# Optimization experiments

Hardware: AMD Instinct MI355X
Metric: run time of the kernel (lower is better)

The kernel has to match this reference:

```python
import jax, jax.numpy as jnp
import numpy as np
from jax import lax

C = 256
HEADS = 8
HEAD_DIM = C // HEADS
B, H, W = 16, 32, 32
EPS = 1e-5


def conv3x3(x, w, b):
    # x: [B,C,H,W], w: [O,I,3,3]
    y = lax.conv_general_dilated(x, w, (1, 1), 'SAME',
                                 dimension_numbers=('NCHW', 'OIHW', 'NCHW'))
    return y + b[None, :, None, None]


def conv1x1(x, w, b):
    # w: [O,C]; pointwise conv as einsum
    return jnp.einsum('oc,bchw->bohw', w, x) + b[None, :, None, None]


def batchnorm(x, gamma, beta, mean, var):
    inv = gamma / jnp.sqrt(var + EPS)
    return x * inv[None, :, None, None] + (beta - mean * inv)[None, :, None, None]


def setup_inputs() -> dict:
    key = jax.random.key(0)
    ks = jax.random.split(key, 16)
    s3 = 1.0 / np.sqrt(C * 9)
    s1 = 1.0 / np.sqrt(C)
    return {
        'x': jax.random.normal(ks[0], (B, C, H, W), jnp.float32),
        'conv1_w': jax.random.normal(ks[1], (C, C, 3, 3), jnp.float32) * s3,
        'conv1_b': jnp.zeros((C,), jnp.float32),
        'bn1_gamma': jnp.ones((C,), jnp.float32),
        'bn1_beta': jnp.zeros((C,), jnp.float32),
        'bn1_mean': jax.random.normal(ks[2], (C,), jnp.float32) * 0.1,
        'bn1_var': jax.random.uniform(ks[3], (C,), jnp.float32, 0.5, 1.5),
        'conv2_w': jax.random.normal(ks[4], (C, C, 3, 3), jnp.float32) * s3,
        'conv2_b': jnp.zeros((C,), jnp.float32),
        'bn2_gamma': jnp.ones((C,), jnp.float32),
        'bn2_beta': jnp.zeros((C,), jnp.float32),
        'bn2_mean': jax.random.normal(ks[5], (C,), jnp.float32) * 0.1,
        'bn2_var': jax.random.uniform(ks[6], (C,), jnp.float32, 0.5, 1.5),
        'q_w': jax.random.normal(ks[7], (C, C), jnp.float32) * s1,
        'q_b': jnp.zeros((C,), jnp.float32),
        'k_w': jax.random.normal(ks[8], (C, C), jnp.float32) * s1,
        'k_b': jnp.zeros((C,), jnp.float32),
        'v_w': jax.random.normal(ks[9], (C, C), jnp.float32) * s1,
        'v_b': jnp.zeros((C,), jnp.float32),
        'out_w': jax.random.normal(ks[10], (C, C), jnp.float32) * s1,
        'out_b': jnp.zeros((C,), jnp.float32),
        'gate': jnp.asarray(0.1, jnp.float32),
    }


def reference(x, conv1_w, conv1_b, bn1_gamma, bn1_beta, bn1_mean, bn1_var,
              conv2_w, conv2_b, bn2_gamma, bn2_beta, bn2_mean, bn2_var,
              q_w, q_b, k_w, k_b, v_w, v_b, out_w, out_b, gate):
    b, c, h, w = x.shape
    n = h * w
    residual = x
    # conv residual path
    conv_out = jax.nn.relu(batchnorm(conv3x3(x, conv1_w, conv1_b),
                                     bn1_gamma, bn1_beta, bn1_mean, bn1_var))
    conv_out = batchnorm(conv3x3(conv_out, conv2_w, conv2_b),
                         bn2_gamma, bn2_beta, bn2_mean, bn2_var)
    # spatial multi-head attention (eval mode: dropout is identity)
    q = conv1x1(x, q_w, q_b).reshape(b, HEADS, HEAD_DIM, n)
    k = conv1x1(x, k_w, k_b).reshape(b, HEADS, HEAD_DIM, n)
    v = conv1x1(x, v_w, v_b).reshape(b, HEADS, HEAD_DIM, n)
    scores = jnp.einsum('bhdn,bhdm->bhnm', q, k) / np.sqrt(HEAD_DIM).astype(np.float32)
    attn = jax.nn.softmax(scores, axis=-1)  # [B,heads,N,N]
    attn_out = jnp.einsum('bhdm,bhnm->bhdn', v, attn).reshape(b, c, h, w)
    attn_out = conv1x1(attn_out, out_w, out_b)
    out = conv_out + jax.nn.sigmoid(gate) * attn_out + residual
    return jax.nn.relu(out)
```

## Files before the change

kernel.cpp:

```cpp
#include <hip/hip_runtime.h>
#include <hip/hip_bf16.h>

using bf16 = __hip_bfloat16;
typedef __attribute__((ext_vector_type(4))) float floatx4;
typedef __attribute__((ext_vector_type(8))) __bf16 bf16x8;
typedef __attribute__((ext_vector_type(4))) __bf16 bf16x4;

#define LGKM_WAIT() asm volatile("s_waitcnt lgkmcnt(0)" ::: "memory")

__device__ __forceinline__ void prep_one(const float* __restrict__ src,
                                         bf16* __restrict__ dst, int idx, int ntaps)
{
    const int kk = idx & 31, o = (idx >> 5) & 255, kc = (idx >> 13) & 7, t = idx >> 16;
    dst[idx] = __float2bfloat16(src[(o * 256 + kc * 32 + kk) * ntaps + t]);
}

__global__ __launch_bounds__(256) void prep_all(
    const float* __restrict__ x,
    const float* __restrict__ w1, const float* __restrict__ w2,
    const float* __restrict__ qw, const float* __restrict__ kw,
    const float* __restrict__ vw, const float* __restrict__ ow,
    bf16* __restrict__ xk, bf16* __restrict__ w1f, bf16* __restrict__ w2f,
    bf16* __restrict__ qwf, bf16* __restrict__ kwf,
    bf16* __restrict__ vwf, bf16* __restrict__ owf)
{
    __shared__ float T[64][65];
    const int blk = blockIdx.x, tid = threadIdx.x;
    if (blk < 1024) {
        const int n0 = (blk & 15) * 64, c0 = ((blk >> 4) & 3) * 64, b = blk >> 6;
        #pragma unroll
        for (int it = 0; it < 4; ++it) {
            const int tau = tid + it * 256;
            const int c = tau >> 4, seg = tau & 15;
            const float4 vv = *(const float4*)&x[((b * 256 + c0 + c) << 10) + n0 + seg * 4];
            T[seg * 4 + 0][c] = vv.x; T[seg * 4 + 1][c] = vv.y;
            T[seg * 4 + 2][c] = vv.z; T[seg * 4 + 3][c] = vv.w;
        }
        __syncthreads();
        #pragma unroll
        for (int it = 0; it < 2; ++it) {
            const int tau = tid + it * 256;
            const int n = tau >> 3, seg = tau & 7;
            bf16x8 o8;
            #pragma unroll
            for (int q = 0; q < 8; ++q) o8[q] = (__bf16)T[n][seg * 8 + q];
            const int c = c0 + seg * 8;
            *(bf16x8*)&xk[((((b << 3) + (c >> 5)) << 10) + n0 + n) * 32 + (c & 31)] = o8;
        }
    } else if (blk < 2176) {
        const int base = (blk - 1024) * 256 + tid;
        #pragma unroll
        for (int k = 0; k < 4; ++k) {
            const int idx = base + k * 294912;
            if (idx < 589824) prep_one(w1, w1f, idx, 9);
            else              prep_one(w2, w2f, idx - 589824, 9);
        }
    } else {
        const int r = (blk - 2176) * 256 + tid;
        prep_one(qw, qwf, r, 1);
        prep_one(kw, kwf, r, 1);
        prep_one(vw, vwf, r, 1);
        prep_one(ow, owf, r, 1);
    }
}

template<int MODE>
__device__ __forceinline__ void conv_body(
    unsigned char* smb, int bn, int bo, int b,
    const bf16* __restrict__ Wf, const bf16* __restrict__ Act,
    const float* __restrict__ bias,
    const float* __restrict__ gam, const float* __restrict__ bet,
    const float* __restrict__ mu, const float* __restrict__ var,
    void* __restrict__ outp)
{
    const int tid = threadIdx.x;
    const int wave = tid >> 6, lane = tid & 63;
    const int quad = lane >> 4, l16 = lane & 15;
    const int wm = wave & 1, wn = wave >> 1;

    int srow[4], scol[4], sn[4]; bool sval[4];
    #pragma unroll
    for (int it = 0; it < 4; ++it) {
        const int s = tid + it * 256;
        const int row = s >> 2;
        const int yi = row / 34, x34 = row - yi * 34;
        const int gy = bn * 4 - 1 + yi, gx = x34 - 1;
        sval[it] = (s < 816) & (gy >= 0) & (gy < 32) & (gx >= 0) & (gx < 32);
        sn[it] = (gy << 5) + gx;
        srow[it] = row; scol[it] = (s & 3) * 8;
    }

    const bf16* __restrict__ act0 = Act + ((size_t)b << 18);
    bf16x8 rg[4];
    #pragma unroll
    for (int it = 0; it < 4; ++it) {
        bf16x8 v = {};
        if (sval[it]) v = *(const bf16x8*)&act0[sn[it] * 32 + scol[it]];
        rg[it] = v;
    }
    {
        bf16* st = (bf16*)smb;
        #pragma unroll
        for (int it = 0; it < 4; ++it)
            if (tid + it * 256 < 816) *(bf16x8*)&st[srow[it] * 40 + scol[it]] = rg[it];
    }
    __syncthreads();

    floatx4 acc[4][2] = {};

    for (int kc = 0; kc < 8; ++kc) {
        if (kc < 7) {
            const bf16* __restrict__ actn = act0 + ((kc + 1) << 15);
            #pragma unroll
            for (int it = 0; it < 4; ++it) {
                bf16x8 v = {};
                if (sval[it]) v = *(const bf16x8*)&actn[sn[it] * 32 + scol[it]];
                rg[it] = v;
            }
        }
        const bf16* __restrict__ cur = (const bf16*)(smb + (kc & 1) * 16320);
        #pragma unroll
        for (int t = 0; t < 9; ++t) {
            const int dy = t / 3 - 1, dx = t % 3 - 1;
            bf16x8 af[4], wf[2];
            #pragma unroll
            for (int p = 0; p < 4; ++p) {
                const int m = wm * 64 + p * 16 + l16;
                const int row = ((m >> 5) + 1 + dy) * 34 + ((m & 31) + 1 + dx);
                af[p] = *(const bf16x8*)&cur[row * 40 + quad * 8];
            }
            #pragma unroll
            for (int p = 0; p < 2; ++p)
                wf[p] = *(const bf16x8*)&Wf[((((t * 8 + kc) << 8) + bo * 64 + wn * 32 + p * 16 + l16) << 5) + quad * 8];
            #pragma unroll
            for (int i = 0; i < 4; ++i)
                #pragma unroll
                for (int j = 0; j < 2; ++j)
                    acc[i][j] = __builtin_amdgcn_mfma_f32_16x16x32_bf16(af[i], wf[j], acc[i][j], 0, 0, 0);
        }
        if (kc < 7) {
            bf16* nxt = (bf16*)(smb + ((kc + 1) & 1) * 16320);
            #pragma unroll
            for (int it = 0; it < 4; ++it)
                if (tid + it * 256 < 816) *(bf16x8*)&nxt[srow[it] * 40 + scol[it]] = rg[it];
        }
        __syncthreads();
    }

    if constexpr (MODE == 0) {
        bf16* rp = (bf16*)(smb + wave * 5120);
        #pragma unroll
        for (int i = 0; i < 4; ++i)
            #pragma unroll
            for (int j = 0; j < 2; ++j) {
                const int oc = bo * 64 + wn * 32 + j * 16 + l16;
                const float inv = gam[oc] * rsqrtf(var[oc] + 1e-5f);
                const float sh = bet[oc] - mu[oc] * inv;
                const float bs = bias[oc];
                #pragma unroll
                for (int r = 0; r < 4; ++r) {
                    const float v = (acc[i][j][r] + bs) * inv + sh;
                    rp[(i * 16 + quad * 4 + r) * 40 + j * 16 + l16] =
                        __float2bfloat16(v < 0.0f ? 0.0f : v);
                }
            }
        LGKM_WAIT();
        const int kc2 = bo * 2 + wn;
        bf16* dst = (bf16*)outp + ((((size_t)b << 3) + kc2) << 15) + (bn * 128 + wm * 64) * 32;
        #pragma unroll
        for (int it = 0; it < 4; ++it) {
            const int s = it * 64 + lane;
            const int nl = s >> 2, cp = (s & 3) * 8;
            *(bf16x8*)&dst[nl * 32 + cp] = *(const bf16x8*)&rp[nl * 40 + cp];
        }
    } else {
        float* rp = (float*)(smb + wave * 8704);
        #pragma unroll
        for (int i = 0; i < 4; ++i)
            #pragma unroll
            for (int j = 0; j < 2; ++j) {
                const int oc = bo * 64 + wn * 32 + j * 16 + l16;
                const float inv = gam[oc] * rsqrtf(var[oc] + 1e-5f);
                const float sh = bet[oc] - mu[oc] * inv;
                const float bs = bias[oc];
                float4 o;
                o.x = (acc[i][j][0] + bs) * inv + sh;
                o.y = (acc[i][j][1] + bs) * inv + sh;
                o.z = (acc[i][j][2] + bs) * inv + sh;
                o.w = (acc[i][j][3] + bs) * inv + sh;
                *(float4*)&rp[(j * 16 + l16) * 68 + i * 16 + quad * 4] = o;
            }
        LGKM_WAIT();
        const int n0 = bn * 128 + wm * 64;
        #pragma unroll
        for (int it = 0; it < 8; ++it) {
            const int s = it * 64 + lane;
            const int ocl = s >> 4, nch = s & 15;
            const int oc = bo * 64 + wn * 32 + ocl;
            float4 v = *(const float4*)&rp[ocl * 68 + nch * 4];
            *(float4*)&((float*)outp)[((b * 256 + oc) << 10) + n0 + nch * 4] = v;
        }
    }
}

__device__ __forceinline__ void qkv_body(
    unsigned char* qsm, int bn, int by, int b,
    const bf16* __restrict__ Wq, const bf16* __restrict__ Wk, const bf16* __restrict__ Wv,
    const bf16* __restrict__ Act,
    const float* __restrict__ bq, const float* __restrict__ bk, const float* __restrict__ bv,
    bf16* __restrict__ Oq, bf16* __restrict__ Ok, bf16* __restrict__ Ov, float qscale)
{
    const int sel = by >> 2, bo = by & 3;
    const bf16* __restrict__ Wf = (sel == 0) ? Wq : (sel == 1) ? Wk : Wv;
    const float* __restrict__ bias = (sel == 0) ? bq : (sel == 1) ? bk : bv;
    const float scale = (sel == 0) ? qscale : 1.0f;

    const int tid = threadIdx.x;
    const int wave = tid >> 6, lane = tid & 63;
    const int quad = lane >> 4, l16 = lane & 15;
    const int wm = wave & 1, wn = wave >> 1;

    floatx4 acc[4][2] = {};

    for (int kc = 0; kc < 8; ++kc) {
        const bf16* __restrict__ actk = Act + ((size_t)b << 18) + (kc << 15);
        bf16x8 af[4], wf[2];
        #pragma unroll
        for (int p = 0; p < 4; ++p)
            af[p] = *(const bf16x8*)&actk[(bn * 128 + wm * 64 + p * 16 + l16) * 32 + quad * 8];
        #pragma unroll
        for (int p = 0; p < 2; ++p)
            wf[p] = *(const bf16x8*)&Wf[(((kc << 8) + bo * 64 + wn * 32 + p * 16 + l16) << 5) + quad * 8];
        #pragma unroll
        for (int i = 0; i < 4; ++i)
            #pragma unroll
            for (int j = 0; j < 2; ++j)
                acc[i][j] = __builtin_amdgcn_mfma_f32_16x16x32_bf16(af[i], wf[j], acc[i][j], 0, 0, 0);
    }

    if (sel < 2) {
        bf16* rp = (bf16*)(qsm + wave * 5120);
        #pragma unroll
        for (int i = 0; i < 4; ++i)
            #pragma unroll
            for (int j = 0; j < 2; ++j) {
                const int oc = bo * 64 + wn * 32 + j * 16 + l16;
                const float bs = bias[oc];
                #pragma unroll
                for (int r = 0; r < 4; ++r)
                    rp[(i * 16 + quad * 4 + r) * 40 + j * 16 + l16] =
                        __float2bfloat16((acc[i][j][r] + bs) * scale);
            }
        LGKM_WAIT();
        bf16* __restrict__ outp = (sel == 0) ? Oq : Ok;
        const int h = bo * 2 + wn;
        bf16* dst = outp + ((((size_t)b << 3) + h) << 15) + (bn * 128 + wm * 64) * 32;
        #pragma unroll
        for (int it = 0; it < 4; ++it) {
            const int s = it * 64 + lane;
            const int nl = s >> 2, cp = (s & 3) * 8;
            *(bf16x8*)&dst[nl * 32 + cp] = *(const bf16x8*)&rp[nl * 40 + cp];
        }
    } else {
        bf16* rp = (bf16*)(qsm + wave * 4608);
        #pragma unroll
        for (int i = 0; i < 4; ++i)
            #pragma unroll
            for (int j = 0; j < 2; ++j) {
                const int oc = bo * 64 + wn * 32 + j * 16 + l16;
                const float bs = bias[oc];
                bf16x4 o4;
                #pragma unroll
                for (int r = 0; r < 4; ++r) o4[r] = (__bf16)(acc[i][j][r] + bs);
                *(bf16x4*)&rp[(j * 16 + l16) * 72 + i * 16 + quad * 4] = o4;
            }
        LGKM_WAIT();
        const int n0 = bn * 128 + wm * 64;
        #pragma unroll
        for (int it = 0; it < 4; ++it) {
            const int s = it * 64 + lane;
            const int ocl = s >> 3, nch = s & 7;
            const int oc = bo * 64 + wn * 32 + ocl;
            *(bf16x8*)&Ov[((b * 256 + oc) << 10) + n0 + nch * 8] =
                *(const bf16x8*)&rp[ocl * 72 + nch * 8];
        }
    }
}

__device__ __forceinline__ void attn_body(
    unsigned char* smb, int L,
    const bf16* __restrict__ Q, const bf16* __restrict__ K,
    const bf16* __restrict__ V, bf16* __restrict__ O)
{
    bf16 (*Pl)[32][136] = (bf16 (*)[32][136])smb;

    const int h = L & 7, slot = L >> 3;
    const int b = slot & 15, qb = slot >> 4;
    const int tid = threadIdx.x;
    const int wave = tid >> 6, lane = tid & 63;
    const int quad = lane >> 4, l16 = lane & 15;

    const bf16* __restrict__ Qh = Q + ((((size_t)b << 3) + h) << 15);
    const bf16* __restrict__ Kh = K + ((((size_t)b << 3) + h) << 15);
    const int qrow0 = qb * 128 + wave * 32;

    bf16x8 qf[2];
    #pragma unroll
    for (int i = 0; i < 2; ++i)
        qf[i] = *(const bf16x8*)&Qh[(qrow0 + i * 16 + l16) * 32 + quad * 8];

    float lp[2] = {0.0f, 0.0f};
    floatx4 oacc[2][2] = {};

    for (int kt = 0; kt < 8; ++kt) {
        bf16x8 kf[8];
        #pragma unroll
        for (int kb = 0; kb < 8; ++kb)
            kf[kb] = *(const bf16x8*)&Kh[(kt * 128 + kb * 16 + l16) * 32 + quad * 8];
        bf16x8 vb[2][4];
        #pragma unroll
        for (int jd = 0; jd < 2; ++jd)
            #pragma unroll
            for (int kk = 0; kk < 4; ++kk)
                vb[jd][kk] = *(const bf16x8*)&V[((b * 256 + h * 32 + jd * 16 + l16) << 10)
                                               + kt * 128 + kk * 32 + quad * 8];

        #pragma unroll
        for (int kb = 0; kb < 8; ++kb) {
            #pragma unroll
            for (int i = 0; i < 2; ++i) {
                floatx4 zz = {0.f, 0.f, 0.f, 0.f};
                floatx4 st = __builtin_amdgcn_mfma_f32_16x16x32_bf16(kf[kb], qf[i], zz, 0, 0, 0);
                const float e0 = __builtin_amdgcn_exp2f(st[0]);
                const float e1 = __builtin_amdgcn_exp2f(st[1]);
                const float e2 = __builtin_amdgcn_exp2f(st[2]);
                const float e3 = __builtin_amdgcn_exp2f(st[3]);
                lp[i] += (e0 + e1) + (e2 + e3);
                bf16x4 p4 = {(__bf16)e0, (__bf16)e1, (__bf16)e2, (__bf16)e3};
                *(bf16x4*)&Pl[wave][i * 16 + l16][kb * 16 + quad * 4] = p4;
            }
        }

        #pragma unroll
        for (int kk = 0; kk < 4; ++kk) {
            bf16x8 pf[2];
            #pragma unroll
            for (int i = 0; i < 2; ++i)
                pf[i] = *(const bf16x8*)&Pl[wave][i * 16 + l16][kk * 32 + quad * 8];
            #pragma unroll
            for (int jd = 0; jd < 2; ++jd)
                #pragma unroll
                for (int i = 0; i < 2; ++i)
                    oacc[jd][i] = __builtin_amdgcn_mfma_f32_16x16x32_bf16(
                        vb[jd][kk], pf[i], oacc[jd][i], 0, 0, 0);
        }
    }

    bf16* __restrict__ Oh = O + ((((size_t)b << 3) + h) << 15);
    #pragma unroll
    for (int i = 0; i < 2; ++i) {
        float l = lp[i];
        l += __shfl_xor(l, 16, 64);
        l += __shfl_xor(l, 32, 64);
        const float inv = 1.0f / l;
        const int qn = qrow0 + i * 16 + l16;
        #pragma unroll
        for (int jd = 0; jd < 2; ++jd) {
            bf16x4 o4;
            #pragma unroll
            for (int r = 0; r < 4; ++r) o4[r] = (__bf16)(oacc[jd][i][r] * inv);
            *(bf16x4*)&Oh[qn * 32 + jd * 16 + quad * 4] = o4;
        }
    }
}

__global__ __launch_bounds__(256) void phase1_k(
    const bf16* __restrict__ w1f, const bf16* __restrict__ xk,
    const float* __restrict__ cb1,
    const float* __restrict__ g1, const float* __restrict__ be1,
    const float* __restrict__ mu1, const float* __restrict__ va1,
    bf16* __restrict__ y1k,
    const bf16* __restrict__ qwf, const bf16* __restrict__ kwf, const bf16* __restrict__ vwf,
    const float* __restrict__ qb_, const float* __restrict__ kb_, const float* __restrict__ vb_,
    bf16* __restrict__ qT, bf16* __restrict__ kT, bf16* __restrict__ vbuf, float qscale)
{
    __shared__ __align__(16) unsigned char smb[34816];
    const int L = blockIdx.x;
    if (L < 512) {
        const int bn = L & 7, bo = (L >> 3) & 3, b = L >> 5;
        conv_body<0>(smb, bn, bo, b, w1f, xk, cb1, g1, be1, mu1, va1, (void*)y1k);
    } else {
        const int L2 = L - 512;
        const int bn = L2 & 7, by = (L2 >> 3) % 12, b = L2 / 96;
        qkv_body(smb, bn, by, b, qwf, kwf, vwf, xk, qb_, kb_, vb_, qT, kT, vbuf, qscale);
    }
}

__global__ __launch_bounds__(256) void phase2_k(
    const bf16* __restrict__ w2f, const bf16* __restrict__ y1k,
    const float* __restrict__ cb2,
    const float* __restrict__ g2, const float* __restrict__ be2,
    const float* __restrict__ mu2, const float* __restrict__ va2,
    float* __restrict__ c2,
    const bf16* __restrict__ qT, const bf16* __restrict__ kT,
    const bf16* __restrict__ vbuf, bf16* __restrict__ attnk)
{
    __shared__ __align__(16) unsigned char smb[34816];
    const int L = blockIdx.x;
    if (L < 512) {
        const int bn = L & 7, bo = (L >> 3) & 3, b = L >> 5;
        conv_body<1>(smb, bn, bo, b, w2f, y1k, cb2, g2, be2, mu2, va2, (void*)c2);
    } else {
        attn_body(smb, L - 512, qT, kT, vbuf, attnk);
    }
}

__global__ __launch_bounds__(256) void fi_k(
    const bf16* __restrict__ Wf, const bf16* __restrict__ Act,
    const float* __restrict__ bias,
    const float* __restrict__ c2, const float* __restrict__ resid,
    const float* __restrict__ gate, float* __restrict__ outp)
{
    __shared__ __align__(16) unsigned char fsm[34816];
    const int bn = blockIdx.x, bo = blockIdx.y, b = blockIdx.z;
    const int tid = threadIdx.x;
    const int wave = tid >> 6, lane = tid & 63;
    const int quad = lane >> 4, l16 = lane & 15;
    const int wm = wave & 1, wn = wave >> 1;

    floatx4 acc[4][2] = {};

    for (int kc = 0; kc < 8; ++kc) {
        const bf16* __restrict__ actk = Act + ((size_t)b << 18) + (kc << 15);
        bf16x8 af[4], wf[2];
        #pragma unroll
        for (int p = 0; p < 4; ++p)
            af[p] = *(const bf16x8*)&actk[(bn * 128 + wm * 64 + p * 16 + l16) * 32 + quad * 8];
        #pragma unroll
        for (int p = 0; p < 2; ++p)
            wf[p] = *(const bf16x8*)&Wf[(((kc << 8) + bo * 64 + wn * 32 + p * 16 + l16) << 5) + quad * 8];
        #pragma unroll
        for (int i = 0; i < 4; ++i)
            #pragma unroll
            for (int j = 0; j < 2; ++j)
                acc[i][j] = __builtin_amdgcn_mfma_f32_16x16x32_bf16(af[i], wf[j], acc[i][j], 0, 0, 0);
    }

    const float sg = 1.0f / (1.0f + __expf(-gate[0]));

    float* rp = (float*)(fsm + wave * 8704);
    #pragma unroll
    for (int i = 0; i < 4; ++i)
        #pragma unroll
        for (int j = 0; j < 2; ++j) {
            const int oc = bo * 64 + wn * 32 + j * 16 + l16;
            const float bs = bias[oc];
            float4 o;
            o.x = acc[i][j][0] + bs; o.y = acc[i][j][1] + bs;
            o.z = acc[i][j][2] + bs; o.w = acc[i][j][3] + bs;
            *(float4*)&rp[(j * 16 + l16) * 68 + i * 16 + quad * 4] = o;
        }
    LGKM_WAIT();
    const int n0 = bn * 128 + wm * 64;
    #pragma unroll
    for (int it = 0; it < 8; ++it) {
        const int s = it * 64 + lane;
        const int ocl = s >> 4, nch = s & 15;
        const int oc = bo * 64 + wn * 32 + ocl;
        const int idx = ((b * 256 + oc) << 10) + n0 + nch * 4;
        float4 v = *(const float4*)&rp[ocl * 68 + nch * 4];
        const float4 cc = *(const float4*)&c2[idx];
        const float4 rr = *(const float4*)&resid[idx];
        float4 o;
        o.x = cc.x + sg * v.x + rr.x; o.y = cc.y + sg * v.y + rr.y;
        o.z = cc.z + sg * v.z + rr.z; o.w = cc.w + sg * v.w + rr.w;
        o.x = o.x < 0.0f ? 0.0f : o.x; o.y = o.y < 0.0f ? 0.0f : o.y;
        o.z = o.z < 0.0f ? 0.0f : o.z; o.w = o.w < 0.0f ? 0.0f : o.w;
        *(float4*)&outp[idx] = o;
    }
}

extern "C" void kernel_launch(void* const* d_in, const int* in_sizes, int n_in,
                              void* d_out, int out_size, void* d_ws, size_t ws_size,
                              hipStream_t stream)
{
    const float* x    = (const float*)d_in[0];
    const float* w1   = (const float*)d_in[1];
    const float* cb1  = (const float*)d_in[2];
    const float* g1   = (const float*)d_in[3];
    const float* be1  = (const float*)d_in[4];
    const float* mu1  = (const float*)d_in[5];
    const float* va1  = (const float*)d_in[6];
    const float* w2   = (const float*)d_in[7];
    const float* cb2  = (const float*)d_in[8];
    const float* g2   = (const float*)d_in[9];
    const float* be2  = (const float*)d_in[10];
    const float* mu2  = (const float*)d_in[11];
    const float* va2  = (const float*)d_in[12];
    const float* qw   = (const float*)d_in[13];
    const float* qb_  = (const float*)d_in[14];
    const float* kw   = (const float*)d_in[15];
    const float* kb_  = (const float*)d_in[16];
    const float* vw   = (const float*)d_in[17];
    const float* vb_  = (const float*)d_in[18];
    const float* ow   = (const float*)d_in[19];
    const float* ob_  = (const float*)d_in[20];
    const float* gate = (const float*)d_in[21];

    char* ws = (char*)d_ws;
    bf16*  xk    = (bf16*) (ws + 0);
    bf16*  y1k   = (bf16*) (ws + 8388608);
    bf16*  attnk = (bf16*) (ws + 8388608);
    float* c2    = (float*)(ws + 16777216);
    bf16*  qT    = (bf16*) (ws + 33554432);
    bf16*  kT    = (bf16*) (ws + 41943040);
    bf16*  vbuf  = (bf16*) (ws + 50331648);
    bf16*  w1f   = (bf16*) (ws + 58720256);
    bf16*  w2f   = (bf16*) (ws + 59899904);
    bf16*  qwf   = (bf16*) (ws + 61079552);
    bf16*  kwf   = (bf16*) (ws + 61210624);
    bf16*  vwf   = (bf16*) (ws + 61341696);
    bf16*  owf   = (bf16*) (ws + 61472768);

    dim3 blk(256, 1, 1);
    prep_all<<<dim3(2432), blk, 0, stream>>>(x, w1, w2, qw, kw, vw, ow,
                                             xk, w1f, w2f, qwf, kwf, vwf, owf);

    phase1_k<<<dim3(2048), blk, 0, stream>>>(w1f, xk, cb1, g1, be1, mu1, va1, y1k,
                                             qwf, kwf, vwf, qb_, kb_, vb_,
                                             qT, kT, vbuf, 0.2550392430300696f);
    phase2_k<<<dim3(1536), blk, 0, stream>>>(w2f, y1k, cb2, g2, be2, mu2, va2, c2,
                                             qT, kT, vbuf, attnk);
    dim3 gg(8, 4, 16);
    fi_k<<<gg, blk, 0, stream>>>(owf, attnk, ob_, c2, x, gate, (float*)d_out);

    (void)in_sizes; (void)n_in; (void)out_size; (void)ws_size;
}
```

Baseline: 241.6 us.

## Move conv2 weight prep into phase1 and store V in attention-tiled layout

```diff
diff --git a/kernel.cpp b/kernel.cpp
--- a/kernel.cpp
+++ b/kernel.cpp
@@ -16,11 +16,10 @@
 }
 
 __global__ __launch_bounds__(256) void prep_all(
-    const float* __restrict__ x,
-    const float* __restrict__ w1, const float* __restrict__ w2,
+    const float* __restrict__ x, const float* __restrict__ w1,
     const float* __restrict__ qw, const float* __restrict__ kw,
     const float* __restrict__ vw, const float* __restrict__ ow,
-    bf16* __restrict__ xk, bf16* __restrict__ w1f, bf16* __restrict__ w2f,
+    bf16* __restrict__ xk, bf16* __restrict__ w1f,
     bf16* __restrict__ qwf, bf16* __restrict__ kwf,
     bf16* __restrict__ vwf, bf16* __restrict__ owf)
 {
@@ -47,16 +46,12 @@
             const int c = c0 + seg * 8;
             *(bf16x8*)&xk[((((b << 3) + (c >> 5)) << 10) + n0 + n) * 32 + (c & 31)] = o8;
         }
-    } else if (blk < 2176) {
-        const int base = (blk - 1024) * 256 + tid;
-        #pragma unroll
-        for (int k = 0; k < 4; ++k) {
-            const int idx = base + k * 294912;
-            if (idx < 589824) prep_one(w1, w1f, idx, 9);
-            else              prep_one(w2, w2f, idx - 589824, 9);
-        }
+    } else if (blk < 1600) {
+        const int base = (blk - 1024) * 1024 + tid;
+        #pragma unroll
+        for (int k = 0; k < 4; ++k) prep_one(w1, w1f, base + k * 256, 9);
     } else {
-        const int r = (blk - 2176) * 256 + tid;
+        const int r = (blk - 1600) * 256 + tid;
         prep_one(qw, qwf, r, 1);
         prep_one(kw, kwf, r, 1);
         prep_one(vw, vwf, r, 1);
@@ -262,28 +257,19 @@
             *(bf16x8*)&dst[nl * 32 + cp] = *(const bf16x8*)&rp[nl * 40 + cp];
         }
     } else {
-        bf16* rp = (bf16*)(qsm + wave * 4608);
         #pragma unroll
         for (int i = 0; i < 4; ++i)
             #pragma unroll
             for (int j = 0; j < 2; ++j) {
                 const int oc = bo * 64 + wn * 32 + j * 16 + l16;
+                const int h = oc >> 5, d = oc & 31;
                 const float bs = bias[oc];
                 bf16x4 o4;
                 #pragma unroll
                 for (int r = 0; r < 4; ++r) o4[r] = (__bf16)(acc[i][j][r] + bs);
-                *(bf16x4*)&rp[(j * 16 + l16) * 72 + i * 16 + quad * 4] = o4;
-            }
-        LGKM_WAIT();
-        const int n0 = bn * 128 + wm * 64;
-        #pragma unroll
-        for (int it = 0; it < 4; ++it) {
-            const int s = it * 64 + lane;
-            const int ocl = s >> 3, nch = s & 7;
-            const int oc = bo * 64 + wn * 32 + ocl;
-            *(bf16x8*)&Ov[((b * 256 + oc) << 10) + n0 + nch * 8] =
-                *(const bf16x8*)&rp[ocl * 72 + nch * 8];
-        }
+                const int key = bn * 128 + wm * 64 + i * 16 + quad * 4;
+                *(bf16x4*)&Ov[(((((size_t)b << 3) + h) * 32 + (key >> 5)) * 32 + d) * 32 + (key & 31)] = o4;
+            }
     }
 }
 
@@ -302,6 +288,7 @@
 
     const bf16* __restrict__ Qh = Q + ((((size_t)b << 3) + h) << 15);
     const bf16* __restrict__ Kh = K + ((((size_t)b << 3) + h) << 15);
+    const bf16* __restrict__ Vh = V + ((((size_t)b << 3) + h) << 15);
     const int qrow0 = qb * 128 + wave * 32;
 
     bf16x8 qf[2];
@@ -322,8 +309,7 @@
         for (int jd = 0; jd < 2; ++jd)
             #pragma unroll
             for (int kk = 0; kk < 4; ++kk)
-                vb[jd][kk] = *(const bf16x8*)&V[((b * 256 + h * 32 + jd * 16 + l16) << 10)
-                                               + kt * 128 + kk * 32 + quad * 8];
+                vb[jd][kk] = *(const bf16x8*)&Vh[(((kt * 4 + kk) << 5) + jd * 16 + l16) * 32 + quad * 8];
 
         #pragma unroll
         for (int kb = 0; kb < 8; ++kb) {
@@ -382,17 +368,22 @@
     bf16* __restrict__ y1k,
     const bf16* __restrict__ qwf, const bf16* __restrict__ kwf, const bf16* __restrict__ vwf,
     const float* __restrict__ qb_, const float* __restrict__ kb_, const float* __restrict__ vb_,
-    bf16* __restrict__ qT, bf16* __restrict__ kT, bf16* __restrict__ vbuf, float qscale)
+    bf16* __restrict__ qT, bf16* __restrict__ kT, bf16* __restrict__ vbuf, float qscale,
+    const float* __restrict__ w2, bf16* __restrict__ w2f)
 {
     __shared__ __align__(16) unsigned char smb[34816];
     const int L = blockIdx.x;
     if (L < 512) {
         const int bn = L & 7, bo = (L >> 3) & 3, b = L >> 5;
         conv_body<0>(smb, bn, bo, b, w1f, xk, cb1, g1, be1, mu1, va1, (void*)y1k);
-    } else {
+    } else if (L < 2048) {
         const int L2 = L - 512;
         const int bn = L2 & 7, by = (L2 >> 3) % 12, b = L2 / 96;
         qkv_body(smb, bn, by, b, qwf, kwf, vwf, xk, qb_, kb_, vb_, qT, kT, vbuf, qscale);
+    } else {
+        const int base = (L - 2048) * 1024 + threadIdx.x;
+        #pragma unroll
+        for (int k = 0; k < 4; ++k) prep_one(w2, w2f, base + k * 256, 9);
     }
 }
 
@@ -523,12 +514,13 @@
     bf16*  owf   = (bf16*) (ws + 61472768);
 
     dim3 blk(256, 1, 1);
-    prep_all<<<dim3(2432), blk, 0, stream>>>(x, w1, w2, qw, kw, vw, ow,
-                                             xk, w1f, w2f, qwf, kwf, vwf, owf);
-
-    phase1_k<<<dim3(2048), blk, 0, stream>>>(w1f, xk, cb1, g1, be1, mu1, va1, y1k,
+    prep_all<<<dim3(1856), blk, 0, stream>>>(x, w1, qw, kw, vw, ow,
+                                             xk, w1f, qwf, kwf, vwf, owf);
+
+    phase1_k<<<dim3(2624), blk, 0, stream>>>(w1f, xk, cb1, g1, be1, mu1, va1, y1k,
                                              qwf, kwf, vwf, qb_, kb_, vb_,
-                                             qT, kT, vbuf, 0.2550392430300696f);
+                                             qT, kT, vbuf, 0.2550392430300696f,
+                                             w2, w2f);
     phase2_k<<<dim3(1536), blk, 0, stream>>>(w2f, y1k, cb2, g2, be2, mu2, va2, c2,
                                              qT, kT, vbuf, attnk);
     dim3 gg(8, 4, 16);
```

Measured after the change: 230.1 us. 4.8% less time.
